# Optimization experiments

Hardware: AMD Instinct MI355X
Metric: run time of the kernel (lower is better)

Reference implementation:

```python
import jax, jax.numpy as jnp
import numpy as np

N_NODES = 50000
N_EDGES = 640000
RANK = 128
ORDER = 3
N_GRAPHS = 50
LN_EPS = 1e-5


def setup_inputs() -> dict:
    key = jax.random.key(0)
    ks = jax.random.split(key, 8)
    features = jax.random.normal(ks[0], (N_NODES, RANK), dtype=jnp.float32)
    src = jax.random.randint(ks[1], (N_EDGES,), 0, N_NODES, dtype=jnp.int32)
    dst = jax.random.randint(ks[2], (N_EDGES,), 0, N_NODES, dtype=jnp.int32)
    batch_num_nodes = jnp.full((N_GRAPHS,), N_NODES // N_GRAPHS, dtype=jnp.int32)
    scale = 1.0 / np.sqrt(RANK)
    Ws = jax.random.normal(ks[3], (ORDER, RANK, RANK), dtype=jnp.float32) * scale
    bs = jnp.zeros((ORDER, RANK), dtype=jnp.float32)
    gammas = jnp.ones((ORDER, RANK), dtype=jnp.float32)
    betas = jnp.zeros((ORDER, RANK), dtype=jnp.float32)
    return {"features": features, "src": src, "dst": dst,
            "batch_num_nodes": batch_num_nodes,
            "Ws": Ws, "bs": bs, "gammas": gammas, "betas": betas}


def _layer_norm(x, gamma, beta):
    mu = jnp.mean(x, axis=-1, keepdims=True)
    var = jnp.mean(jnp.square(x - mu), axis=-1, keepdims=True)
    return (x - mu) * jax.lax.rsqrt(var + LN_EPS) * gamma + beta


def reference(features, src, dst, batch_num_nodes, Ws, bs, gammas, betas):
    ones = jnp.ones((src.shape[0],), dtype=features.dtype)
    deg_out = jax.ops.segment_sum(ones, src, num_segments=N_NODES)  # out-degree of src nodes
    deg_in = jax.ops.segment_sum(ones, dst, num_segments=N_NODES)   # in-degree of dst nodes
    inv_sqrt_out = jax.lax.rsqrt(jnp.maximum(deg_out, 1.0))[:, None]
    inv_sqrt_in = jax.lax.rsqrt(jnp.maximum(deg_in, 1.0))[:, None]

    feats = features
    for i in range(ORDER):
        # DGL GraphConv, norm='both': h = D_in^{-1/2} A D_out^{-1/2} (X W) + b
        h = (feats @ Ws[i]) * inv_sqrt_out
        agg = jax.ops.segment_sum(h[src], dst, num_segments=N_NODES)
        h = agg * inv_sqrt_in + bs[i]
        h = _layer_norm(h, gammas[i], betas[i])
        feats = jax.nn.relu(h)  # dropout is identity at inference

    first_idx = jnp.cumsum(jnp.concatenate([jnp.zeros((1,), jnp.int32), batch_num_nodes[:-1]]))
    return feats[first_idx]
```

## Files before the change

### kernel.cpp

```cpp
#include <hip/hip_runtime.h>

#define RANK 128
#define LN_EPS 1e-5f

#define NCH 4
#define CHUNK 12800
#define BINS (NCH * CHUNK)
#define ECH 64
#define BT 1024
#define BMWL ((BINS + 31) / 32)

using short8 = __attribute__((ext_vector_type(8))) short;
using v4f    = __attribute__((ext_vector_type(4))) float;

__device__ inline unsigned short f2bf(float f) {
    unsigned u = __float_as_uint(f);
    unsigned r = (u + 0x7FFF + ((u >> 16) & 1)) >> 16;
    return (unsigned short)r;
}

__global__ __launch_bounds__(BT) void hist_part(const int* __restrict__ src,
                                                const int* __restrict__ dst,
                                                unsigned short* __restrict__ pdst,
                                                unsigned short* __restrict__ psrc,
                                                const float* __restrict__ Ws,
                                                short* __restrict__ Wt, int nE) {
    int c = blockIdx.x, n = blockIdx.y, z = blockIdx.z;
    if (c == ECH) {
        int sid = (n + 4 * z) * BT + threadIdx.x;
        if (sid < 3 * 2048) {
            int l = sid >> 11;
            int s = sid & 2047;
            int lane = s & 63, ct = (s >> 6) & 7, k0 = s >> 9;
            int m = lane & 15, quad = lane >> 4;
            const float* W = Ws + (size_t)l * RANK * RANK;
            short* o = Wt + (size_t)l * 16384 + (size_t)s * 8;
#pragma unroll
            for (int j = 0; j < 8; j++)
                o[j] = (short)f2bf(W[(k0 * 32 + quad * 8 + j) * RANK + ct * 16 + m]);
        }
        return;
    }
    __shared__ int h[CHUNK];
    const int* arr = z ? src : dst;
    unsigned short* pout = z ? psrc : pdst;
    int base = n * CHUNK;
    for (int i = threadIdx.x; i < CHUNK; i += BT) h[i] = 0;
    __syncthreads();
    int epc = (nE + ECH - 1) / ECH;
    int e0 = c * epc, e1 = min(e0 + epc, nE);
    int tid = threadIdx.x;
    int a0 = min((e0 + 3) & ~3, e1);
    if (tid < a0 - e0) {
        int v = arr[e0 + tid] - base;
        if ((unsigned)v < (unsigned)CHUNK) atomicAdd(&h[v], 1);
    }
    int rem = e1 - a0;
    int nv = (rem > 0) ? (rem & ~3) : 0;
    for (int e = a0 + tid * 4; e < a0 + nv; e += BT * 4) {
        int4 v4 = *(const int4*)(arr + e);
        int v;
        v = v4.x - base; if ((unsigned)v < (unsigned)CHUNK) atomicAdd(&h[v], 1);
        v = v4.y - base; if ((unsigned)v < (unsigned)CHUNK) atomicAdd(&h[v], 1);
        v = v4.z - base; if ((unsigned)v < (unsigned)CHUNK) atomicAdd(&h[v], 1);
        v = v4.w - base; if ((unsigned)v < (unsigned)CHUNK) atomicAdd(&h[v], 1);
    }
    int t0 = a0 + nv;
    if (tid < e1 - t0) {
        int v = arr[t0 + tid] - base;
        if ((unsigned)v < (unsigned)CHUNK) atomicAdd(&h[v], 1);
    }
    __syncthreads();
    unsigned short* o = pout + (size_t)c * BINS + base;
    for (int i = threadIdx.x; i < CHUNK; i += BT) o[i] = (unsigned short)h[i];
}

__global__ __launch_bounds__(256) void reduce_scan1(const unsigned short* __restrict__ pdst,
                                                    const unsigned short* __restrict__ psrc,
                                                    int* __restrict__ counts,
                                                    float* __restrict__ invin,
                                                    float* __restrict__ invout,
                                                    int* __restrict__ ends,
                                                    int* __restrict__ bsums, int M) {
    __shared__ int tmp[256];
    int tid = threadIdx.x;
    int gid = blockIdx.x * 256 + tid;
    int cd = 0, cs = 0;
    if (gid < M) {
#pragma unroll 8
        for (int c = 0; c < ECH; c++) {
            cd += pdst[(size_t)c * BINS + gid];
            cs += psrc[(size_t)c * BINS + gid];
        }
        counts[gid] = cd;
        invin[gid]  = rsqrtf(fmaxf((float)cd, 1.0f));
        invout[gid] = rsqrtf(fmaxf((float)cs, 1.0f));
    }
    tmp[tid] = cd;
    __syncthreads();
    for (int off = 1; off < 256; off <<= 1) {
        int t = (tid >= off) ? tmp[tid - off] : 0;
        __syncthreads();
        tmp[tid] += t;
        __syncthreads();
    }
    if (gid < M) ends[gid] = tmp[tid];
    if (tid == 255) bsums[blockIdx.x] = tmp[255];
}

__global__ __launch_bounds__(256) void scan23_offs(int* __restrict__ ends,
                                                   const int* __restrict__ counts,
                                                   const int* __restrict__ bsums,
                                                   const unsigned short* __restrict__ pdst,
                                                   int* __restrict__ pcur, int nb, int M) {
    __shared__ int red[256];
    int tid = threadIdx.x;
    int b = blockIdx.x;
    red[tid] = (tid < b && tid < nb) ? bsums[tid] : 0;
    __syncthreads();
    for (int off = 128; off > 0; off >>= 1) {
        if (tid < off) red[tid] += red[tid + off];
        __syncthreads();
    }
    int prefix = red[0];
    int gid = b * 256 + tid;
    if (gid < M) {
        int e = ends[gid] + prefix;
        ends[gid] = e;
        int run = e - counts[gid];
#pragma unroll 8
        for (int c = 0; c < ECH; c++) {
            size_t idx = (size_t)c * BINS + gid;
            int t = pdst[idx];
            pcur[idx] = run;
            run += t;
        }
    }
}

__global__ __launch_bounds__(BT) void fill_sorted(const int* __restrict__ src,
                                                  const int* __restrict__ dst,
                                                  const int* __restrict__ pcur,
                                                  int* __restrict__ csr_src, int nE) {
    __shared__ int cur[CHUNK];
    int c = blockIdx.x, n = blockIdx.y;
    int base = n * CHUNK;
    const int* o = pcur + (size_t)c * BINS + base;
    for (int i = threadIdx.x; i < CHUNK; i += BT) cur[i] = o[i];
    __syncthreads();
    int epc = (nE + ECH - 1) / ECH;
    int e0 = c * epc, e1 = min(e0 + epc, nE);
    int tid = threadIdx.x;
    int a0 = min((e0 + 3) & ~3, e1);
    if (tid < a0 - e0) {
        int e = e0 + tid;
        int d = dst[e] - base;
        if ((unsigned)d < (unsigned)CHUNK) csr_src[atomicAdd(&cur[d], 1)] = src[e];
    }
    int rem = e1 - a0;
    int nv = (rem > 0) ? (rem & ~3) : 0;
    for (int e = a0 + tid * 4; e < a0 + nv; e += BT * 4) {
        int4 d4 = *(const int4*)(dst + e);
        int4 s4 = *(const int4*)(src + e);
        int d;
        d = d4.x - base; if ((unsigned)d < (unsigned)CHUNK) csr_src[atomicAdd(&cur[d], 1)] = s4.x;
        d = d4.y - base; if ((unsigned)d < (unsigned)CHUNK) csr_src[atomicAdd(&cur[d], 1)] = s4.y;
        d = d4.z - base; if ((unsigned)d < (unsigned)CHUNK) csr_src[atomicAdd(&cur[d], 1)] = s4.z;
        d = d4.w - base; if ((unsigned)d < (unsigned)CHUNK) csr_src[atomicAdd(&cur[d], 1)] = s4.w;
    }
    int t0 = a0 + nv;
    if (tid < e1 - t0) {
        int e = t0 + tid;
        int d = dst[e] - base;
        if ((unsigned)d < (unsigned)CHUNK) csr_src[atomicAdd(&cur[d], 1)] = src[e];
    }
}

__global__ __launch_bounds__(256) void mark_expand3(const int* __restrict__ bnn, int nG,
                                                    const int* __restrict__ ends,
                                                    const int* __restrict__ csr_src,
                                                    int* __restrict__ T3, int* __restrict__ cnt3,
                                                    int* __restrict__ T2, int* __restrict__ cnt2) {
    __shared__ unsigned bm[BMWL];
    __shared__ int lcnt;
    int tid = threadIdx.x;
    for (int i = tid; i < BMWL; i += 256) bm[i] = 0;
    if (tid == 0) lcnt = 0;
    __syncthreads();
    if (tid < 64) {
        int lane = tid;
        if (nG <= 64) {
            int v = (lane < nG) ? bnn[lane] : 0;
            int orig = v;
#pragma unroll
            for (int off = 1; off < 64; off <<= 1) {
                int t = __shfl_up(v, off);
                if (lane >= off) v += t;
            }
            int excl = v - orig;
            if (lane < nG) T3[lane] = excl;
            if (lane == 0) *cnt3 = nG;
        } else if (lane == 0) {
            int idx = 0;
            for (int g = 0; g < nG; g++) { T3[g] = idx; idx += bnn[g]; }
            *cnt3 = nG;
        }
    }
    __syncthreads();
    int lane = tid & 63, w = tid >> 6;
    for (int i = w; i < nG; i += 4) {
        int node = T3[i];
        int end = ends[node];
        int beg = (node == 0) ? 0 : ends[node - 1];
        for (int e0 = beg; e0 < end; e0 += 64) {
            if (e0 + lane < end) {
                int u = csr_src[e0 + lane];
                unsigned old = atomicOr(&bm[u >> 5], 1u << (u & 31));
                if (!((old >> (u & 31)) & 1)) {
                    int pos = atomicAdd(&lcnt, 1);
                    T2[pos] = u;
                }
            }
        }
    }
    __syncthreads();
    if (tid == 0) *cnt2 = lcnt;
}

__global__ __launch_bounds__(256) void frontier_csr(const int* __restrict__ list,
                                                    const int* __restrict__ cnt,
                                                    const int* __restrict__ ends,
                                                    const int* __restrict__ csr_src,
                                                    unsigned* __restrict__ bm_out,
                                                    int* __restrict__ out_list,
                                                    int* __restrict__ out_cnt) {
    int lane = threadIdx.x & 63;
    int wg = blockIdx.x * 4 + (threadIdx.x >> 6);
    int nW = gridDim.x * 4;
    int n = *cnt;
    for (int i = wg; i < n; i += nW) {
        int node = list[i];
        int end = ends[node];
        int beg = (node == 0) ? 0 : ends[node - 1];
        for (int e0 = beg; e0 < end; e0 += 64) {
            int u = 0;
            bool flag = false;
            if (e0 + lane < end) {
                u = csr_src[e0 + lane];
                unsigned old = atomicOr(&bm_out[u >> 5], 1u << (u & 31));
                flag = !((old >> (u & 31)) & 1);
            }
            unsigned long long mask = __ballot(flag);
            if (mask) {
                int leader = __ffsll((long long)mask) - 1;
                int base = 0;
                if (lane == leader) base = atomicAdd(out_cnt, __popcll(mask));
                base = __shfl(base, leader);
                if (flag) out_list[base + __popcll(mask & ((1ull << lane) - 1))] = u;
            }
        }
    }
}

template <int LAST, int FP32IN>
__global__ __launch_bounds__(256) void layer_fused(const void* __restrict__ FinV,
                                                   const float* __restrict__ edge_scale,
                                                   const int* __restrict__ ends,
                                                   const int* __restrict__ csr_src,
                                                   const short* __restrict__ Wt,
                                                   const float* __restrict__ invin,
                                                   const float* __restrict__ invout,
                                                   const float* __restrict__ bias,
                                                   const float* __restrict__ gamma,
                                                   const float* __restrict__ beta,
                                                   const int* __restrict__ list,
                                                   const int* __restrict__ cnt,
                                                   unsigned short* __restrict__ Fout,
                                                   float* __restrict__ out) {
    const unsigned* Fb = (const unsigned*)FinV;
    const float4*  Ff = (const float4*)FinV;
    __shared__ short As[16][136];
    __shared__ float sstat[2][4][16];
    __shared__ float sinv[2][16];
    __shared__ int snode[16];
    int tid = threadIdx.x;
    int w = tid >> 6, lane = tid & 63;
    int seg = lane >> 4, m = lane & 15;
    int n = *cnt;
    int tiles = (n + 15) >> 4;

    float bb[2], gg[2], pp[2];
#pragma unroll
    for (int j = 0; j < 2; j++) {
        int col = (w * 2 + j) * 16 + m;
        bb[j] = bias[col]; gg[j] = gamma[col]; pp[j] = beta[col];
    }

    for (int t = blockIdx.x; t < tiles; t += gridDim.x) {
        int base = t * 16;

        for (int q = 0; q < 4; q++) {
            int rr = w * 4 + q;
            int gr = base + rr;
            float ax[8];
#pragma unroll
            for (int k = 0; k < 8; k++) ax[k] = 0.f;
            int node = -1;
            if (gr < n) {
                node = list[gr];
                int end = ends[node];
                int e = (node == 0) ? 0 : ends[node - 1];
                while (e < end) {
                    int rem = end - e;
                    int myi = 0;
                    if (lane < rem) myi = csr_src[e + lane];
                    int nn = min(rem, 64);
                    int p = 0;
                    for (; p + 16 <= nn; p += 16) {
                        if (FP32IN) {
                            float4 fa[4], fb4[4]; float so[4];
#pragma unroll
                            for (int gi = 0; gi < 4; gi++) {
                                int idx = __shfl(myi, p + gi * 4 + seg);
                                so[gi] = edge_scale[idx];
                                const float4* qq = Ff + (size_t)idx * 32 + m * 2;
                                fa[gi] = qq[0]; fb4[gi] = qq[1];
                            }
#pragma unroll
                            for (int gi = 0; gi < 4; gi++) {
                                ax[0] += fa[gi].x * so[gi]; ax[1] += fa[gi].y * so[gi];
                                ax[2] += fa[gi].z * so[gi]; ax[3] += fa[gi].w * so[gi];
                                ax[4] += fb4[gi].x * so[gi]; ax[5] += fb4[gi].y * so[gi];
                                ax[6] += fb4[gi].z * so[gi]; ax[7] += fb4[gi].w * so[gi];
                            }
                        } else {
                            uint4 u[4];
#pragma unroll
                            for (int gi = 0; gi < 4; gi++) {
                                int idx = __shfl(myi, p + gi * 4 + seg);
                                u[gi] = *(const uint4*)(Fb + (size_t)idx * 64 + m * 4);
                            }
#pragma unroll
                            for (int gi = 0; gi < 4; gi++) {
                                ax[0] += __uint_as_float(u[gi].x << 16);
                                ax[1] += __uint_as_float(u[gi].x & 0xFFFF0000u);
                                ax[2] += __uint_as_float(u[gi].y << 16);
                                ax[3] += __uint_as_float(u[gi].y & 0xFFFF0000u);
                                ax[4] += __uint_as_float(u[gi].z << 16);
                                ax[5] += __uint_as_float(u[gi].z & 0xFFFF0000u);
                                ax[6] += __uint_as_float(u[gi].w << 16);
                                ax[7] += __uint_as_float(u[gi].w & 0xFFFF0000u);
                            }
                        }
                    }
                    for (; p < nn; p += 4) {
                        bool act = (p + seg) < nn;
                        int idx = __shfl(myi, (p + seg) & 63);
                        if (act) {
                            if (FP32IN) {
                                float so = edge_scale[idx];
                                const float4* qq = Ff + (size_t)idx * 32 + m * 2;
                                float4 fa = qq[0], fb4 = qq[1];
                                ax[0] += fa.x * so; ax[1] += fa.y * so;
                                ax[2] += fa.z * so; ax[3] += fa.w * so;
                                ax[4] += fb4.x * so; ax[5] += fb4.y * so;
                                ax[6] += fb4.z * so; ax[7] += fb4.w * so;
                            } else {
                                uint4 u = *(const uint4*)(Fb + (size_t)idx * 64 + m * 4);
                                ax[0] += __uint_as_float(u.x << 16);
                                ax[1] += __uint_as_float(u.x & 0xFFFF0000u);
                                ax[2] += __uint_as_float(u.y << 16);
                                ax[3] += __uint_as_float(u.y & 0xFFFF0000u);
                                ax[4] += __uint_as_float(u.z << 16);
                                ax[5] += __uint_as_float(u.z & 0xFFFF0000u);
                                ax[6] += __uint_as_float(u.w << 16);
                                ax[7] += __uint_as_float(u.w & 0xFFFF0000u);
                            }
                        }
                    }
                    e += nn;
                }
#pragma unroll
                for (int k = 0; k < 8; k++) {
                    ax[k] += __shfl_xor(ax[k], 16);
                    ax[k] += __shfl_xor(ax[k], 32);
                }
            }
            if (seg == 0) {
                uint4 o;
                o.x = (unsigned)f2bf(ax[0]) | ((unsigned)f2bf(ax[1]) << 16);
                o.y = (unsigned)f2bf(ax[2]) | ((unsigned)f2bf(ax[3]) << 16);
                o.z = (unsigned)f2bf(ax[4]) | ((unsigned)f2bf(ax[5]) << 16);
                o.w = (unsigned)f2bf(ax[6]) | ((unsigned)f2bf(ax[7]) << 16);
                *(uint4*)&As[rr][8 * m] = o;
            }
            if (lane == 0) {
                snode[rr] = node;
                sinv[0][rr] = (node >= 0) ? invin[node] : 1.f;
                sinv[1][rr] = (node >= 0) ? invout[node] : 1.f;
            }
        }
        __syncthreads();

        short8 a[4];
#pragma unroll
        for (int k0 = 0; k0 < 4; k0++)
            a[k0] = *(const short8*)&As[m][k0 * 32 + seg * 8];
        v4f acc[2];
        acc[0] = (v4f){0.f, 0.f, 0.f, 0.f};
        acc[1] = (v4f){0.f, 0.f, 0.f, 0.f};
#pragma unroll
        for (int k0 = 0; k0 < 4; k0++) {
#pragma unroll
            for (int j = 0; j < 2; j++) {
                int ct = w * 2 + j;
                short8 b = *(const short8*)(Wt + (size_t)((k0 * 8 + ct) * 64 + lane) * 8);
                acc[j] = __builtin_amdgcn_mfma_f32_16x16x32_bf16(a[k0], b, acc[j], 0, 0, 0);
            }
        }

        float x[4][2];
#pragma unroll
        for (int r = 0; r < 4; r++) {
            int row = seg * 4 + r;
            float iv = sinv[0][row];
            float s = 0.f, sq = 0.f;
#pragma unroll
            for (int j = 0; j < 2; j++) {
                float c = acc[j][r] * iv + bb[j];
                x[r][j] = c;
                s += c; sq += c * c;
            }
#pragma unroll
            for (int off = 1; off < 16; off <<= 1) {
                s  += __shfl_xor(s, off);
                sq += __shfl_xor(sq, off);
            }
            if (m == 0) { sstat[0][w][row] = s; sstat[1][w][row] = sq; }
        }
        __syncthreads();

#pragma unroll
        for (int r = 0; r < 4; r++) {
            int row = seg * 4 + r;
            int gr = base + row;
            if (gr >= n) continue;
            float s  = sstat[0][0][row] + sstat[0][1][row] + sstat[0][2][row] + sstat[0][3][row];
            float sq = sstat[1][0][row] + sstat[1][1][row] + sstat[1][2][row] + sstat[1][3][row];
            float mu = s * (1.0f / RANK);
            float var = sq * (1.0f / RANK) - mu * mu;
            float rs = rsqrtf(var + LN_EPS);
#pragma unroll
            for (int j = 0; j < 2; j++) {
                int col = (w * 2 + j) * 16 + m;
                float y = fmaxf((x[r][j] - mu) * rs * gg[j] + pp[j], 0.f);
                if (LAST) {
                    out[(size_t)gr * RANK + col] = y;
                } else {
                    Fout[(size_t)snode[row] * RANK + col] = f2bf(y * sinv[1][row]);
                }
            }
        }
        __syncthreads();
    }
}

extern "C" void kernel_launch(void* const* d_in, const int* in_sizes, int n_in,
                              void* d_out, int out_size, void* d_ws, size_t ws_size,
                              hipStream_t stream) {
    const float* features = (const float*)d_in[0];
    const int* src = (const int*)d_in[1];
    const int* dst = (const int*)d_in[2];
    const int* bnn = (const int*)d_in[3];
    const float* Ws = (const float*)d_in[4];
    const float* bs = (const float*)d_in[5];
    const float* gammas = (const float*)d_in[6];
    const float* betas = (const float*)d_in[7];
    float* out = (float*)d_out;

    int M  = in_sizes[0] / RANK;
    int nE = in_sizes[1];
    int nG = in_sizes[3];
    int bmw = (M + 31) / 32;

    char* ws = (char*)d_ws;
    size_t off = 0;
    auto alloc = [&](size_t bytes) {
        void* p = ws + off;
        off += (bytes + 255) & ~(size_t)255;
        return p;
    };
    int*   counts  = (int*)alloc((size_t)M * 4);
    int*   ends    = (int*)alloc((size_t)M * 4);
    int*   bsums   = (int*)alloc(256 * 4);
    float* invout  = (float*)alloc((size_t)M * 4);
    float* invin   = (float*)alloc((size_t)M * 4);
    int*   csr_src = (int*)alloc((size_t)nE * 4);
    short* Wt      = (short*)alloc((size_t)3 * 16384 * 2);
    short* F1      = (short*)alloc((size_t)M * RANK * 2);
    short* F2      = (short*)alloc((size_t)M * RANK * 2);
    unsigned short* pdst = (unsigned short*)alloc((size_t)ECH * BINS * 2);
    unsigned short* psrc = (unsigned short*)alloc((size_t)ECH * BINS * 2);
    int*   pcur    = (int*)alloc((size_t)ECH * BINS * 4);
    char*  zbase   = (char*)alloc((size_t)(bmw + 1) * 4);
    unsigned* bm1  = (unsigned*)zbase;
    int*   cnt1    = (int*)(bm1 + bmw);
    int*   cnt2    = (int*)alloc(256);
    int*   cnt3    = (int*)alloc(256);
    int*   T3      = (int*)alloc((size_t)((nG + 63) & ~63) * 4);
    int*   T2      = (int*)alloc((size_t)M * 4);
    int*   T1      = (int*)alloc((size_t)M * 4);

    int nb = (M + 255) / 256;

    hipMemsetAsync(zbase, 0, (size_t)(bmw + 1) * 4, stream);

    hist_part<<<dim3(ECH + 1, NCH, 2), BT, 0, stream>>>(src, dst, pdst, psrc, Ws, Wt, nE);
    reduce_scan1<<<nb, 256, 0, stream>>>(pdst, psrc, counts, invin, invout, ends, bsums, M);
    scan23_offs<<<nb, 256, 0, stream>>>(ends, counts, bsums, pdst, pcur, nb, M);
    fill_sorted<<<dim3(ECH, NCH), BT, 0, stream>>>(src, dst, pcur, csr_src, nE);

    mark_expand3<<<1, 256, 0, stream>>>(bnn, nG, ends, csr_src, T3, cnt3, T2, cnt2);
    frontier_csr<<<64, 256, 0, stream>>>(T2, cnt2, ends, csr_src, bm1, T1, cnt1);

    layer_fused<0, 1><<<512, 256, 0, stream>>>(features, invout, ends, csr_src, Wt,
                                               invin, invout, bs, gammas, betas,
                                               T1, cnt1, (unsigned short*)F1, nullptr);
    layer_fused<0, 0><<<64, 256, 0, stream>>>(F1, nullptr, ends, csr_src, Wt + 16384,
                                              invin, invout, bs + RANK, gammas + RANK, betas + RANK,
                                              T2, cnt2, (unsigned short*)F2, nullptr);
    layer_fused<1, 0><<<(nG + 15) / 16, 256, 0, stream>>>(F2, nullptr, ends, csr_src, Wt + 32768,
                                                          invin, invout, bs + 2 * RANK,
                                                          gammas + 2 * RANK, betas + 2 * RANK,
                                                          T3, cnt3, nullptr, out);
}
```

Before: 178.1 us.

## Replace global CSR sort with per-level frontier edge filtering and compact CSRs

Instead of building a full dst-sorted CSR over all edges via histogram, scan and scatter, the pipeline now builds only a src-degree histogram. It then filters the edge list level by level, using bitmaps of the needed destination nodes, into small compacted per-level CSRs with slot-indexed features. This avoids the dst histogram, the two scan kernels and the full scatter. In exchange it rescans the whole edge list three times and relies on single-block build_level kernels and a fixed BMWMAX shared-memory bitmap that caps the node count.

```diff
diff --git a/kernel.cpp b/kernel.cpp
--- a/kernel.cpp
+++ b/kernel.cpp
@@ -8,7 +8,8 @@
 #define BINS (NCH * CHUNK)
 #define ECH 64
 #define BT 1024
-#define BMWL ((BINS + 31) / 32)
+#define BMWMAX 1600
+#define NSB 96
 
 using short8 = __attribute__((ext_vector_type(8))) short;
 using v4f    = __attribute__((ext_vector_type(4))) float;
@@ -19,15 +20,55 @@
     return (unsigned short)r;
 }
 
-__global__ __launch_bounds__(BT) void hist_part(const int* __restrict__ src,
-                                                const int* __restrict__ dst,
-                                                unsigned short* __restrict__ pdst,
+__global__ __launch_bounds__(BT) void hist_mark(const int* __restrict__ src,
+                                                const float* __restrict__ Ws,
+                                                short* __restrict__ Wt,
+                                                const int* __restrict__ bnn, int nG,
                                                 unsigned short* __restrict__ psrc,
-                                                const float* __restrict__ Ws,
-                                                short* __restrict__ Wt, int nE) {
-    int c = blockIdx.x, n = blockIdx.y, z = blockIdx.z;
-    if (c == ECH) {
-        int sid = (n + 4 * z) * BT + threadIdx.x;
+                                                int* __restrict__ T3, int* __restrict__ map3,
+                                                unsigned* __restrict__ bm3,
+                                                int* __restrict__ mcnt3, int* __restrict__ cnt3,
+                                                int nE, int M) {
+    __shared__ int h[CHUNK];
+    int c = blockIdx.x, n = blockIdx.y;
+    int tid = threadIdx.x;
+    if (c >= ECH) {
+        int which = c - ECH;
+        if (which == 1 && n == 3) {
+            int bmw = (M + 31) / 32;
+            for (int i = tid; i < bmw; i += BT) bm3[i] = 0;
+            __syncthreads();
+            if (tid < 64) {
+                int lane = tid;
+                if (nG <= 64) {
+                    int v = (lane < nG) ? bnn[lane] : 0;
+                    int orig = v;
+#pragma unroll
+                    for (int off = 1; off < 64; off <<= 1) {
+                        int t = __shfl_up(v, off);
+                        if (lane >= off) v += t;
+                    }
+                    int excl = v - orig;
+                    if (lane < nG) {
+                        T3[lane] = excl;
+                        map3[excl] = lane;
+                        atomicOr(&bm3[excl >> 5], 1u << (excl & 31));
+                    }
+                } else if (lane == 0) {
+                    int idx = 0;
+                    for (int g = 0; g < nG; g++) {
+                        T3[g] = idx; map3[idx] = g;
+                        atomicOr(&bm3[idx >> 5], 1u << (idx & 31));
+                        idx += bnn[g];
+                    }
+                }
+            }
+            if (tid == 0) { *mcnt3 = 0; *cnt3 = nG; }
+            return;
+        }
+        int sid;
+        if (which == 0) sid = n * BT + tid;
+        else { if (n >= 2) return; sid = 4096 + n * BT + tid; }
         if (sid < 3 * 2048) {
             int l = sid >> 11;
             int s = sid & 2047;
@@ -41,24 +82,20 @@
         }
         return;
     }
-    __shared__ int h[CHUNK];
-    const int* arr = z ? src : dst;
-    unsigned short* pout = z ? psrc : pdst;
     int base = n * CHUNK;
-    for (int i = threadIdx.x; i < CHUNK; i += BT) h[i] = 0;
+    for (int i = tid; i < CHUNK; i += BT) h[i] = 0;
     __syncthreads();
     int epc = (nE + ECH - 1) / ECH;
     int e0 = c * epc, e1 = min(e0 + epc, nE);
-    int tid = threadIdx.x;
     int a0 = min((e0 + 3) & ~3, e1);
     if (tid < a0 - e0) {
-        int v = arr[e0 + tid] - base;
+        int v = src[e0 + tid] - base;
         if ((unsigned)v < (unsigned)CHUNK) atomicAdd(&h[v], 1);
     }
     int rem = e1 - a0;
     int nv = (rem > 0) ? (rem & ~3) : 0;
     for (int e = a0 + tid * 4; e < a0 + nv; e += BT * 4) {
-        int4 v4 = *(const int4*)(arr + e);
+        int4 v4 = *(const int4*)(src + e);
         int v;
         v = v4.x - base; if ((unsigned)v < (unsigned)CHUNK) atomicAdd(&h[v], 1);
         v = v4.y - base; if ((unsigned)v < (unsigned)CHUNK) atomicAdd(&h[v], 1);
@@ -67,198 +104,199 @@
     }
     int t0 = a0 + nv;
     if (tid < e1 - t0) {
-        int v = arr[t0 + tid] - base;
+        int v = src[t0 + tid] - base;
         if ((unsigned)v < (unsigned)CHUNK) atomicAdd(&h[v], 1);
     }
     __syncthreads();
-    unsigned short* o = pout + (size_t)c * BINS + base;
-    for (int i = threadIdx.x; i < CHUNK; i += BT) o[i] = (unsigned short)h[i];
-}
-
-__global__ __launch_bounds__(256) void reduce_scan1(const unsigned short* __restrict__ pdst,
-                                                    const unsigned short* __restrict__ psrc,
-                                                    int* __restrict__ counts,
-                                                    float* __restrict__ invin,
-                                                    float* __restrict__ invout,
-                                                    int* __restrict__ ends,
-                                                    int* __restrict__ bsums, int M) {
-    __shared__ int tmp[256];
+    unsigned short* o = psrc + (size_t)c * BINS + base;
+    for (int i = tid; i < CHUNK; i += BT) o[i] = (unsigned short)h[i];
+}
+
+template <int COUNT>
+__device__ void scan_match_body(const int* __restrict__ src, const int* __restrict__ dst,
+                                const unsigned* __restrict__ bm, int2* __restrict__ E,
+                                int* __restrict__ mcnt, int* __restrict__ gcount,
+                                const int* __restrict__ mapPrev,
+                                int nE, int bid, int nblocks, int M) {
+    __shared__ unsigned bmL[BMWMAX];
     int tid = threadIdx.x;
-    int gid = blockIdx.x * 256 + tid;
-    int cd = 0, cs = 0;
-    if (gid < M) {
-#pragma unroll 8
-        for (int c = 0; c < ECH; c++) {
-            cd += pdst[(size_t)c * BINS + gid];
-            cs += psrc[(size_t)c * BINS + gid];
-        }
-        counts[gid] = cd;
-        invin[gid]  = rsqrtf(fmaxf((float)cd, 1.0f));
-        invout[gid] = rsqrtf(fmaxf((float)cs, 1.0f));
-    }
-    tmp[tid] = cd;
-    __syncthreads();
-    for (int off = 1; off < 256; off <<= 1) {
-        int t = (tid >= off) ? tmp[tid - off] : 0;
-        __syncthreads();
-        tmp[tid] += t;
-        __syncthreads();
-    }
-    if (gid < M) ends[gid] = tmp[tid];
-    if (tid == 255) bsums[blockIdx.x] = tmp[255];
-}
-
-__global__ __launch_bounds__(256) void scan23_offs(int* __restrict__ ends,
-                                                   const int* __restrict__ counts,
-                                                   const int* __restrict__ bsums,
-                                                   const unsigned short* __restrict__ pdst,
-                                                   int* __restrict__ pcur, int nb, int M) {
-    __shared__ int red[256];
-    int tid = threadIdx.x;
-    int b = blockIdx.x;
-    red[tid] = (tid < b && tid < nb) ? bsums[tid] : 0;
-    __syncthreads();
-    for (int off = 128; off > 0; off >>= 1) {
-        if (tid < off) red[tid] += red[tid + off];
-        __syncthreads();
-    }
-    int prefix = red[0];
-    int gid = b * 256 + tid;
-    if (gid < M) {
-        int e = ends[gid] + prefix;
-        ends[gid] = e;
-        int run = e - counts[gid];
-#pragma unroll 8
-        for (int c = 0; c < ECH; c++) {
-            size_t idx = (size_t)c * BINS + gid;
-            int t = pdst[idx];
-            pcur[idx] = run;
-            run += t;
-        }
-    }
-}
-
-__global__ __launch_bounds__(BT) void fill_sorted(const int* __restrict__ src,
-                                                  const int* __restrict__ dst,
-                                                  const int* __restrict__ pcur,
-                                                  int* __restrict__ csr_src, int nE) {
-    __shared__ int cur[CHUNK];
-    int c = blockIdx.x, n = blockIdx.y;
-    int base = n * CHUNK;
-    const int* o = pcur + (size_t)c * BINS + base;
-    for (int i = threadIdx.x; i < CHUNK; i += BT) cur[i] = o[i];
-    __syncthreads();
-    int epc = (nE + ECH - 1) / ECH;
-    int e0 = c * epc, e1 = min(e0 + epc, nE);
-    int tid = threadIdx.x;
-    int a0 = min((e0 + 3) & ~3, e1);
-    if (tid < a0 - e0) {
-        int e = e0 + tid;
-        int d = dst[e] - base;
-        if ((unsigned)d < (unsigned)CHUNK) csr_src[atomicAdd(&cur[d], 1)] = src[e];
-    }
-    int rem = e1 - a0;
-    int nv = (rem > 0) ? (rem & ~3) : 0;
-    for (int e = a0 + tid * 4; e < a0 + nv; e += BT * 4) {
-        int4 d4 = *(const int4*)(dst + e);
-        int4 s4 = *(const int4*)(src + e);
-        int d;
-        d = d4.x - base; if ((unsigned)d < (unsigned)CHUNK) csr_src[atomicAdd(&cur[d], 1)] = s4.x;
-        d = d4.y - base; if ((unsigned)d < (unsigned)CHUNK) csr_src[atomicAdd(&cur[d], 1)] = s4.y;
-        d = d4.z - base; if ((unsigned)d < (unsigned)CHUNK) csr_src[atomicAdd(&cur[d], 1)] = s4.z;
-        d = d4.w - base; if ((unsigned)d < (unsigned)CHUNK) csr_src[atomicAdd(&cur[d], 1)] = s4.w;
-    }
-    int t0 = a0 + nv;
-    if (tid < e1 - t0) {
-        int e = t0 + tid;
-        int d = dst[e] - base;
-        if ((unsigned)d < (unsigned)CHUNK) csr_src[atomicAdd(&cur[d], 1)] = src[e];
-    }
-}
-
-__global__ __launch_bounds__(256) void mark_expand3(const int* __restrict__ bnn, int nG,
-                                                    const int* __restrict__ ends,
-                                                    const int* __restrict__ csr_src,
-                                                    int* __restrict__ T3, int* __restrict__ cnt3,
-                                                    int* __restrict__ T2, int* __restrict__ cnt2) {
-    __shared__ unsigned bm[BMWL];
-    __shared__ int lcnt;
-    int tid = threadIdx.x;
-    for (int i = tid; i < BMWL; i += 256) bm[i] = 0;
-    if (tid == 0) lcnt = 0;
-    __syncthreads();
-    if (tid < 64) {
-        int lane = tid;
-        if (nG <= 64) {
-            int v = (lane < nG) ? bnn[lane] : 0;
-            int orig = v;
-#pragma unroll
-            for (int off = 1; off < 64; off <<= 1) {
-                int t = __shfl_up(v, off);
-                if (lane >= off) v += t;
-            }
-            int excl = v - orig;
-            if (lane < nG) T3[lane] = excl;
-            if (lane == 0) *cnt3 = nG;
-        } else if (lane == 0) {
-            int idx = 0;
-            for (int g = 0; g < nG; g++) { T3[g] = idx; idx += bnn[g]; }
-            *cnt3 = nG;
-        }
-    }
-    __syncthreads();
-    int lane = tid & 63, w = tid >> 6;
-    for (int i = w; i < nG; i += 4) {
-        int node = T3[i];
-        int end = ends[node];
-        int beg = (node == 0) ? 0 : ends[node - 1];
-        for (int e0 = beg; e0 < end; e0 += 64) {
-            if (e0 + lane < end) {
-                int u = csr_src[e0 + lane];
-                unsigned old = atomicOr(&bm[u >> 5], 1u << (u & 31));
-                if (!((old >> (u & 31)) & 1)) {
-                    int pos = atomicAdd(&lcnt, 1);
-                    T2[pos] = u;
-                }
-            }
-        }
-    }
-    __syncthreads();
-    if (tid == 0) *cnt2 = lcnt;
-}
-
-__global__ __launch_bounds__(256) void frontier_csr(const int* __restrict__ list,
-                                                    const int* __restrict__ cnt,
-                                                    const int* __restrict__ ends,
-                                                    const int* __restrict__ csr_src,
-                                                    unsigned* __restrict__ bm_out,
-                                                    int* __restrict__ out_list,
-                                                    int* __restrict__ out_cnt) {
-    int lane = threadIdx.x & 63;
-    int wg = blockIdx.x * 4 + (threadIdx.x >> 6);
-    int nW = gridDim.x * 4;
-    int n = *cnt;
-    for (int i = wg; i < n; i += nW) {
-        int node = list[i];
-        int end = ends[node];
-        int beg = (node == 0) ? 0 : ends[node - 1];
-        for (int e0 = beg; e0 < end; e0 += 64) {
-            int u = 0;
-            bool flag = false;
-            if (e0 + lane < end) {
-                u = csr_src[e0 + lane];
-                unsigned old = atomicOr(&bm_out[u >> 5], 1u << (u & 31));
-                flag = !((old >> (u & 31)) & 1);
-            }
+    int bmw = (M + 31) / 32;
+    for (int i = tid; i < bmw; i += BT) bmL[i] = bm[i];
+    __syncthreads();
+    int lane = tid & 63;
+    long long stride = (long long)nblocks * BT * 4;
+    for (long long b0 = ((long long)bid * BT + tid) * 4; b0 < nE; b0 += stride) {
+        int dv[4], sv[4]; int c4;
+        if (b0 + 4 <= nE) {
+            int4 d4 = *(const int4*)(dst + b0);
+            int4 s4 = *(const int4*)(src + b0);
+            dv[0] = d4.x; dv[1] = d4.y; dv[2] = d4.z; dv[3] = d4.w;
+            sv[0] = s4.x; sv[1] = s4.y; sv[2] = s4.z; sv[3] = s4.w;
+            c4 = 4;
+        } else {
+            c4 = (int)(nE - b0);
+            for (int j = 0; j < c4; j++) { dv[j] = dst[b0 + j]; sv[j] = src[b0 + j]; }
+        }
+#pragma unroll
+        for (int j = 0; j < 4; j++) {
+            bool flag = (j < c4) && ((bmL[dv[j] >> 5] >> (dv[j] & 31)) & 1);
+            if (COUNT && flag) atomicAdd(&gcount[mapPrev[dv[j]]], 1);
             unsigned long long mask = __ballot(flag);
             if (mask) {
                 int leader = __ffsll((long long)mask) - 1;
-                int base = 0;
-                if (lane == leader) base = atomicAdd(out_cnt, __popcll(mask));
-                base = __shfl(base, leader);
-                if (flag) out_list[base + __popcll(mask & ((1ull << lane) - 1))] = u;
-            }
-        }
+                int pos0 = 0;
+                if (lane == leader) pos0 = atomicAdd(mcnt, __popcll(mask));
+                pos0 = __shfl(pos0, leader);
+                if (flag) E[pos0 + __popcll(mask & ((1ull << lane) - 1))] = make_int2(sv[j], dv[j]);
+            }
+        }
+    }
+}
+
+__global__ __launch_bounds__(BT) void reduce_scan3(const unsigned short* __restrict__ psrc,
+                                                   float* __restrict__ invout, int M, int nbR,
+                                                   const int* __restrict__ src,
+                                                   const int* __restrict__ dst,
+                                                   const unsigned* __restrict__ bm3,
+                                                   int2* __restrict__ E3, int* __restrict__ mcnt3,
+                                                   int nE) {
+    if ((int)blockIdx.x < nbR) {
+        int gid = blockIdx.x * BT + threadIdx.x;
+        if (gid < M) {
+            int cs = 0;
+#pragma unroll 8
+            for (int c = 0; c < ECH; c++) cs += psrc[(size_t)c * BINS + gid];
+            invout[gid] = rsqrtf(fmaxf((float)cs, 1.0f));
+        }
+        return;
+    }
+    scan_match_body<0>(src, dst, bm3, E3, mcnt3, nullptr, nullptr, nE,
+                       blockIdx.x - nbR, gridDim.x - nbR, M);
+}
+
+template <int COUNT>
+__global__ __launch_bounds__(BT) void scan_match(const int* __restrict__ src,
+                                                 const int* __restrict__ dst,
+                                                 const unsigned* __restrict__ bm,
+                                                 int2* __restrict__ E, int* __restrict__ mcnt,
+                                                 int* __restrict__ gcount,
+                                                 const int* __restrict__ mapPrev, int nE, int M) {
+    scan_match_body<COUNT>(src, dst, bm, E, mcnt, gcount, mapPrev, nE,
+                           blockIdx.x, gridDim.x, M);
+}
+
+__global__ __launch_bounds__(BT) void build_level(const int2* __restrict__ E,
+                                                  const int* __restrict__ mcnt,
+                                                  const int* __restrict__ mapPrev,
+                                                  const int* __restrict__ cntPrev,
+                                                  const float* __restrict__ invout,
+                                                  int* __restrict__ Tnew, int* __restrict__ mapNew,
+                                                  int* __restrict__ cntNew, float* __restrict__ soNew,
+                                                  int* __restrict__ csrPrev, int* __restrict__ endsPrev,
+                                                  float* __restrict__ invinPrev,
+                                                  unsigned* __restrict__ bmNew,
+                                                  int* __restrict__ mcntNext,
+                                                  int* __restrict__ gzero, int M) {
+    __shared__ unsigned bmL[BMWMAX];
+    __shared__ int cntL[CHUNK];
+    __shared__ int tmp[BT];
+    __shared__ int lcnt;
+    int tid = threadIdx.x;
+    int bmw = (M + 31) / 32;
+    int m = *mcnt;
+    int nPrev = *cntPrev;
+    for (int i = tid; i < bmw; i += BT) bmL[i] = 0;
+    for (int i = tid; i < nPrev; i += BT) cntL[i] = 0;
+    if (tid == 0) lcnt = 0;
+    __syncthreads();
+    for (int i = tid; i < m; i += BT) {
+        int2 e = E[i];
+        int u = e.x;
+        unsigned old = atomicOr(&bmL[u >> 5], 1u << (u & 31));
+        if (!((old >> (u & 31)) & 1)) {
+            int sl = atomicAdd(&lcnt, 1);
+            Tnew[sl] = u;
+            mapNew[u] = sl;
+            soNew[sl] = invout[u];
+        }
+        atomicAdd(&cntL[mapPrev[e.y]], 1);
+    }
+    __syncthreads();
+    int carry = 0;
+    for (int c0 = 0; c0 < nPrev; c0 += BT) {
+        int v = (c0 + tid < nPrev) ? cntL[c0 + tid] : 0;
+        __syncthreads();
+        tmp[tid] = v;
+        __syncthreads();
+        for (int off = 1; off < BT; off <<= 1) {
+            int t = (tid >= off) ? tmp[tid - off] : 0;
+            __syncthreads();
+            tmp[tid] += t;
+            __syncthreads();
+        }
+        int incl = tmp[tid] + carry;
+        int tot = tmp[BT - 1];
+        if (c0 + tid < nPrev) {
+            endsPrev[c0 + tid] = incl;
+            invinPrev[c0 + tid] = rsqrtf(fmaxf((float)v, 1.0f));
+            cntL[c0 + tid] = incl - v;
+        }
+        carry += tot;
+    }
+    __syncthreads();
+    for (int i = tid; i < m; i += BT) {
+        int2 e = E[i];
+        int pos = atomicAdd(&cntL[mapPrev[e.y]], 1);
+        csrPrev[pos] = mapNew[e.x];
+    }
+    __syncthreads();
+    for (int i = tid; i < bmw; i += BT) bmNew[i] = bmL[i];
+    int L = lcnt;
+    if (gzero) for (int i = tid; i < L; i += BT) gzero[i] = 0;
+    if (tid == 0) { *cntNew = L; *mcntNext = 0; }
+}
+
+__global__ __launch_bounds__(BT) void cursors_kernel(const int* __restrict__ gcount,
+                                                     const int* __restrict__ cnt1,
+                                                     int* __restrict__ ends1,
+                                                     float* __restrict__ invin1,
+                                                     int* __restrict__ gcursor) {
+    __shared__ int tmp[BT];
+    int tid = threadIdx.x;
+    int n1 = *cnt1;
+    int carry = 0;
+    for (int c0 = 0; c0 < n1; c0 += BT) {
+        int v = (c0 + tid < n1) ? gcount[c0 + tid] : 0;
+        __syncthreads();
+        tmp[tid] = v;
+        __syncthreads();
+        for (int off = 1; off < BT; off <<= 1) {
+            int t = (tid >= off) ? tmp[tid - off] : 0;
+            __syncthreads();
+            tmp[tid] += t;
+            __syncthreads();
+        }
+        int incl = tmp[tid] + carry;
+        int tot = tmp[BT - 1];
+        if (c0 + tid < n1) {
+            ends1[c0 + tid] = incl;
+            invin1[c0 + tid] = rsqrtf(fmaxf((float)v, 1.0f));
+            gcursor[c0 + tid] = incl - v;
+        }
+        carry += tot;
+    }
+}
+
+__global__ __launch_bounds__(BT) void fill1_kernel(const int2* __restrict__ E1,
+                                                   const int* __restrict__ mcnt1,
+                                                   const int* __restrict__ map1,
+                                                   int* __restrict__ gcursor,
+                                                   int* __restrict__ csr1) {
+    int m = *mcnt1;
+    for (int i = blockIdx.x * BT + threadIdx.x; i < m; i += gridDim.x * BT) {
+        int2 e = E1[i];
+        int pos = atomicAdd(&gcursor[map1[e.y]], 1);
+        csr1[pos] = e.x;
     }
 }
 
@@ -266,14 +304,13 @@
 __global__ __launch_bounds__(256) void layer_fused(const void* __restrict__ FinV,
                                                    const float* __restrict__ edge_scale,
                                                    const int* __restrict__ ends,
-                                                   const int* __restrict__ csr_src,
+                                                   const int* __restrict__ csr,
                                                    const short* __restrict__ Wt,
-                                                   const float* __restrict__ invin,
-                                                   const float* __restrict__ invout,
+                                                   const float* __restrict__ invin_slot,
+                                                   const float* __restrict__ so_slot,
                                                    const float* __restrict__ bias,
                                                    const float* __restrict__ gamma,
                                                    const float* __restrict__ beta,
-                                                   const int* __restrict__ list,
                                                    const int* __restrict__ cnt,
                                                    unsigned short* __restrict__ Fout,
                                                    float* __restrict__ out) {
@@ -282,7 +319,6 @@
     __shared__ short As[16][136];
     __shared__ float sstat[2][4][16];
     __shared__ float sinv[2][16];
-    __shared__ int snode[16];
     int tid = threadIdx.x;
     int w = tid >> 6, lane = tid & 63;
     int seg = lane >> 4, m = lane & 15;
@@ -305,15 +341,13 @@
             float ax[8];
 #pragma unroll
             for (int k = 0; k < 8; k++) ax[k] = 0.f;
-            int node = -1;
             if (gr < n) {
-                node = list[gr];
-                int end = ends[node];
-                int e = (node == 0) ? 0 : ends[node - 1];
+                int end = ends[gr];
+                int e = (gr == 0) ? 0 : ends[gr - 1];
                 while (e < end) {
                     int rem = end - e;
                     int myi = 0;
-                    if (lane < rem) myi = csr_src[e + lane];
+                    if (lane < rem) myi = csr[e + lane];
                     int nn = min(rem, 64);
                     int p = 0;
                     for (; p + 16 <= nn; p += 16) {
@@ -395,9 +429,8 @@
                 *(uint4*)&As[rr][8 * m] = o;
             }
             if (lane == 0) {
-                snode[rr] = node;
-                sinv[0][rr] = (node >= 0) ? invin[node] : 1.f;
-                sinv[1][rr] = (node >= 0) ? invout[node] : 1.f;
+                sinv[0][rr] = (gr < n) ? invin_slot[gr] : 1.f;
+                sinv[1][rr] = (LAST || gr >= n) ? 1.f : so_slot[gr];
             }
         }
         __syncthreads();
@@ -454,11 +487,8 @@
             for (int j = 0; j < 2; j++) {
                 int col = (w * 2 + j) * 16 + m;
                 float y = fmaxf((x[r][j] - mu) * rs * gg[j] + pp[j], 0.f);
-                if (LAST) {
-                    out[(size_t)gr * RANK + col] = y;
-                } else {
-                    Fout[(size_t)snode[row] * RANK + col] = f2bf(y * sinv[1][row]);
-                }
+                if (LAST) out[(size_t)gr * RANK + col] = y;
+                else Fout[(size_t)gr * RANK + col] = f2bf(y * sinv[1][row]);
             }
         }
         __syncthreads();
@@ -481,7 +511,6 @@
     int M  = in_sizes[0] / RANK;
     int nE = in_sizes[1];
     int nG = in_sizes[3];
-    int bmw = (M + 31) / 32;
 
     char* ws = (char*)d_ws;
     size_t off = 0;
@@ -490,47 +519,65 @@
         off += (bytes + 255) & ~(size_t)255;
         return p;
     };
-    int*   counts  = (int*)alloc((size_t)M * 4);
-    int*   ends    = (int*)alloc((size_t)M * 4);
-    int*   bsums   = (int*)alloc(256 * 4);
+    unsigned short* psrc = (unsigned short*)alloc((size_t)ECH * BINS * 2);
+    short* Wt      = (short*)alloc((size_t)3 * 16384 * 2);
     float* invout  = (float*)alloc((size_t)M * 4);
-    float* invin   = (float*)alloc((size_t)M * 4);
-    int*   csr_src = (int*)alloc((size_t)nE * 4);
-    short* Wt      = (short*)alloc((size_t)3 * 16384 * 2);
-    short* F1      = (short*)alloc((size_t)M * RANK * 2);
-    short* F2      = (short*)alloc((size_t)M * RANK * 2);
-    unsigned short* pdst = (unsigned short*)alloc((size_t)ECH * BINS * 2);
-    unsigned short* psrc = (unsigned short*)alloc((size_t)ECH * BINS * 2);
-    int*   pcur    = (int*)alloc((size_t)ECH * BINS * 4);
-    char*  zbase   = (char*)alloc((size_t)(bmw + 1) * 4);
-    unsigned* bm1  = (unsigned*)zbase;
-    int*   cnt1    = (int*)(bm1 + bmw);
-    int*   cnt2    = (int*)alloc(256);
-    int*   cnt3    = (int*)alloc(256);
+    int*   map3    = (int*)alloc((size_t)M * 4);
+    int*   map2    = (int*)alloc((size_t)M * 4);
+    int*   map1    = (int*)alloc((size_t)M * 4);
     int*   T3      = (int*)alloc((size_t)((nG + 63) & ~63) * 4);
     int*   T2      = (int*)alloc((size_t)M * 4);
     int*   T1      = (int*)alloc((size_t)M * 4);
-
-    int nb = (M + 255) / 256;
-
-    hipMemsetAsync(zbase, 0, (size_t)(bmw + 1) * 4, stream);
-
-    hist_part<<<dim3(ECH + 1, NCH, 2), BT, 0, stream>>>(src, dst, pdst, psrc, Ws, Wt, nE);
-    reduce_scan1<<<nb, 256, 0, stream>>>(pdst, psrc, counts, invin, invout, ends, bsums, M);
-    scan23_offs<<<nb, 256, 0, stream>>>(ends, counts, bsums, pdst, pcur, nb, M);
-    fill_sorted<<<dim3(ECH, NCH), BT, 0, stream>>>(src, dst, pcur, csr_src, nE);
-
-    mark_expand3<<<1, 256, 0, stream>>>(bnn, nG, ends, csr_src, T3, cnt3, T2, cnt2);
-    frontier_csr<<<64, 256, 0, stream>>>(T2, cnt2, ends, csr_src, bm1, T1, cnt1);
-
-    layer_fused<0, 1><<<512, 256, 0, stream>>>(features, invout, ends, csr_src, Wt,
-                                               invin, invout, bs, gammas, betas,
-                                               T1, cnt1, (unsigned short*)F1, nullptr);
-    layer_fused<0, 0><<<64, 256, 0, stream>>>(F1, nullptr, ends, csr_src, Wt + 16384,
-                                              invin, invout, bs + RANK, gammas + RANK, betas + RANK,
-                                              T2, cnt2, (unsigned short*)F2, nullptr);
-    layer_fused<1, 0><<<(nG + 15) / 16, 256, 0, stream>>>(F2, nullptr, ends, csr_src, Wt + 32768,
-                                                          invin, invout, bs + 2 * RANK,
+    float* so2     = (float*)alloc((size_t)M * 4);
+    float* so1     = (float*)alloc((size_t)M * 4);
+    float* invin3  = (float*)alloc((size_t)((nG + 63) & ~63) * 4);
+    float* invin2  = (float*)alloc((size_t)M * 4);
+    float* invin1  = (float*)alloc((size_t)M * 4);
+    int*   ends3   = (int*)alloc((size_t)((nG + 63) & ~63) * 4);
+    int*   ends2   = (int*)alloc((size_t)M * 4);
+    int*   ends1   = (int*)alloc((size_t)M * 4);
+    int*   csr3    = (int*)alloc((size_t)nE * 4);
+    int*   csr2    = (int*)alloc((size_t)nE * 4);
+    int*   csr1    = (int*)alloc((size_t)nE * 4);
+    int2*  E3      = (int2*)alloc((size_t)nE * 8);
+    int2*  E2      = (int2*)alloc((size_t)nE * 8);
+    int2*  E1      = (int2*)alloc((size_t)nE * 8);
+    unsigned* bm3  = (unsigned*)alloc(BMWMAX * 4);
+    unsigned* bm2  = (unsigned*)alloc(BMWMAX * 4);
+    unsigned* bm1  = (unsigned*)alloc(BMWMAX * 4);
+    int*   mcnt3   = (int*)alloc(256);
+    int*   mcnt2   = (int*)alloc(256);
+    int*   mcnt1   = (int*)alloc(256);
+    int*   cnt3    = (int*)alloc(256);
+    int*   cnt2    = (int*)alloc(256);
+    int*   cnt1    = (int*)alloc(256);
+    int*   gcount  = (int*)alloc((size_t)M * 4);
+    int*   gcursor = (int*)alloc((size_t)M * 4);
+    short* F1      = (short*)alloc((size_t)M * RANK * 2);
+    short* F2      = (short*)alloc((size_t)M * RANK * 2);
+
+    int nbR = (M + BT - 1) / BT;
+
+    hist_mark<<<dim3(ECH + 2, NCH), BT, 0, stream>>>(src, Ws, Wt, bnn, nG, psrc,
+                                                     T3, map3, bm3, mcnt3, cnt3, nE, M);
+    reduce_scan3<<<nbR + NSB, BT, 0, stream>>>(psrc, invout, M, nbR, src, dst, bm3, E3, mcnt3, nE);
+    build_level<<<1, BT, 0, stream>>>(E3, mcnt3, map3, cnt3, invout, T2, map2, cnt2, so2,
+                                      csr3, ends3, invin3, bm2, mcnt2, nullptr, M);
+    scan_match<0><<<NSB, BT, 0, stream>>>(src, dst, bm2, E2, mcnt2, nullptr, nullptr, nE, M);
+    build_level<<<1, BT, 0, stream>>>(E2, mcnt2, map2, cnt2, invout, T1, map1, cnt1, so1,
+                                      csr2, ends2, invin2, bm1, mcnt1, gcount, M);
+    scan_match<1><<<NSB, BT, 0, stream>>>(src, dst, bm1, E1, mcnt1, gcount, map1, nE, M);
+    cursors_kernel<<<1, BT, 0, stream>>>(gcount, cnt1, ends1, invin1, gcursor);
+    fill1_kernel<<<32, BT, 0, stream>>>(E1, mcnt1, map1, gcursor, csr1);
+
+    layer_fused<0, 1><<<512, 256, 0, stream>>>(features, invout, ends1, csr1, Wt,
+                                               invin1, so1, bs, gammas, betas, cnt1,
+                                               (unsigned short*)F1, nullptr);
+    layer_fused<0, 0><<<64, 256, 0, stream>>>(F1, nullptr, ends2, csr2, Wt + 16384,
+                                              invin2, so2, bs + RANK, gammas + RANK, betas + RANK,
+                                              cnt2, (unsigned short*)F2, nullptr);
+    layer_fused<1, 0><<<(nG + 15) / 16, 256, 0, stream>>>(F2, nullptr, ends3, csr3, Wt + 32768,
+                                                          invin3, nullptr, bs + 2 * RANK,
                                                           gammas + 2 * RANK, betas + 2 * RANK,
-                                                          T3, cnt3, nullptr, out);
-}
+                                                          cnt3, nullptr, out);
+}
```

After: 397.9 us. 2.23x slower.
